# Kernel optimization log

Hardware: AMD Instinct MI355X
Metric: run time of the kernel (lower is better)

Reference implementation:

```python
import jax, jax.numpy as jnp
import numpy as np

B, N, DIN, DOUT, E, K = 64, 883, 2, 64, 10, 2
CIN = DIN + DOUT


def _dgcn(x, node_emb, time, day, speed, occupy,
          fc1_w, fc1_b, fc2_w, fc2_b, fc3_w, fc3_b, wpool, bpool):
    # x: (B, N, C); node_emb: (N, E); time/day/speed/occupy: (B, N, E)
    n = x.shape[1]
    # hyper-network filter from input features
    h = jax.nn.sigmoid(x @ fc1_w + fc1_b)
    h = jax.nn.sigmoid(h @ fc2_w + fc2_b)
    filt = h @ fc3_w + fc3_b                                  # (B, N, E)
    # dynamic node embedding: static emb modulated by time/day/speed/occupy embeddings
    dyn = node_emb[None] * time * day * speed * occupy        # (B, N, E)
    nodevec = jnp.tanh(dyn * filt)                            # (B, N, E)
    A = jax.nn.relu(jnp.einsum('bne,bme->bnm', nodevec, nodevec))  # (B, N, N)
    d = jnp.sum(A, axis=-1) ** -0.5                           # (B, N)
    I = jnp.eye(n, dtype=x.dtype)
    L = I[None] - A * d[:, :, None] * d[:, None, :]           # normalized laplacian support
    # cheb_k = 2 supports: identity and L
    x_g = jnp.stack([x, jnp.einsum('bnm,bmc->bnc', L, x)], axis=2)  # (B, N, K, C)
    weights = jnp.einsum('ne,ekio->nkio', node_emb, wpool)    # (N, K, C, O)
    bias = node_emb @ bpool                                   # (N, O)
    return jnp.einsum('bnki,nkio->bno', x_g, weights) + bias[None]


def setup_inputs() -> dict:
    key = jax.random.key(0)
    ks = jax.random.split(key, 23)
    rn = lambda k, s, sc=1.0: jax.random.normal(k, s, dtype=jnp.float32) * sc
    return dict(
        x=rn(ks[0], (B, N, DIN)),
        state=rn(ks[1], (B, N, DOUT), 0.1),
        node_embeddings=rn(ks[2], (N, E)),
        time=rn(ks[3], (B, N, E), 0.5),
        day=rn(ks[4], (B, N, E), 0.5),
        speed=rn(ks[5], (B, N, E), 0.5),
        occupy=rn(ks[6], (B, N, E), 0.5),
        gate_wpool=rn(ks[7], (E, K, CIN, 2 * DOUT), 0.1),
        gate_bpool=rn(ks[8], (E, 2 * DOUT), 0.1),
        gate_fc1_w=rn(ks[9], (CIN, 16), 0.1), gate_fc1_b=rn(ks[10], (16,), 0.1),
        gate_fc2_w=rn(ks[11], (16, 2), 0.1), gate_fc2_b=rn(ks[12], (2,), 0.1),
        gate_fc3_w=rn(ks[13], (2, E), 0.1), gate_fc3_b=rn(ks[14], (E,), 0.1),
        update_wpool=rn(ks[15], (E, K, CIN, DOUT), 0.1),
        update_bpool=rn(ks[16], (E, DOUT), 0.1),
        update_fc1_w=rn(ks[17], (CIN, 16), 0.1), update_fc1_b=rn(ks[18], (16,), 0.1),
        update_fc2_w=rn(ks[19], (16, 2), 0.1), update_fc2_b=rn(ks[20], (2,), 0.1),
        update_fc3_w=rn(ks[21], (2, E), 0.1), update_fc3_b=rn(ks[22], (E,), 0.1),
    )


def reference(x, state, node_embeddings, time, day, speed, occupy,
              gate_wpool, gate_bpool, gate_fc1_w, gate_fc1_b, gate_fc2_w,
              gate_fc2_b, gate_fc3_w, gate_fc3_b,
              update_wpool, update_bpool, update_fc1_w, update_fc1_b,
              update_fc2_w, update_fc2_b, update_fc3_w, update_fc3_b):
    xs = jnp.concatenate([x, state], axis=-1)                 # (B, N, DIN+DOUT)
    z_r = jax.nn.sigmoid(_dgcn(xs, node_embeddings, time, day, speed, occupy,
                               gate_fc1_w, gate_fc1_b, gate_fc2_w, gate_fc2_b,
                               gate_fc3_w, gate_fc3_b, gate_wpool, gate_bpool))
    z, r = jnp.split(z_r, 2, axis=-1)
    cand = jnp.concatenate([x, z * state], axis=-1)
    hc = jnp.tanh(_dgcn(cand, node_embeddings, time, day, speed, occupy,
                        update_fc1_w, update_fc1_b, update_fc2_w, update_fc2_b,
                        update_fc3_w, update_fc3_b, update_wpool, update_bpool))
    return r * state + (1.0 - r) * hc
```

## Files before the change

kernel.cpp:

```cpp
#include <hip/hip_runtime.h>
#include <cmath>

#define BB 64
#define NN 883
#define NP 896
#define EE 10
#define CC 66
#define KP 160

typedef __attribute__((ext_vector_type(8))) short bf16x8;
typedef __attribute__((ext_vector_type(4))) float f32x4;

__device__ __forceinline__ float sigmoidf_(float v) { return 1.f / (1.f + expf(-v)); }

__device__ __forceinline__ unsigned short f2bf(float f) {
  unsigned int u = __float_as_uint(f);
  u = u + 0x7FFFu + ((u >> 16) & 1u);
  return (unsigned short)(u >> 16);
}
__device__ __forceinline__ float bf2f(unsigned short h) {
  return __uint_as_float(((unsigned int)h) << 16);
}

template<int PHASE>
__global__ __launch_bounds__(256) void k1_hyper(
    const float* __restrict__ x, const float* __restrict__ state,
    const float* __restrict__ zr, const float* __restrict__ emb,
    const float* __restrict__ tme, const float* __restrict__ day,
    const float* __restrict__ spd, const float* __restrict__ occ,
    const float* __restrict__ w1, const float* __restrict__ b1,
    const float* __restrict__ w2, const float* __restrict__ b2,
    const float* __restrict__ w3, const float* __restrict__ b3,
    unsigned short* __restrict__ Acat, unsigned short* __restrict__ nvP) {
  int idx = blockIdx.x * 256 + threadIdx.x;
  if (idx >= BB * NP) return;
  int b = idx / NP, n = idx - b * NP;
  if (n >= NN) {
    *(uint4*)&nvP[(size_t)idx * 16] = make_uint4(0, 0, 0, 0);
    *(uint4*)&nvP[(size_t)idx * 16 + 8] = make_uint4(0, 0, 0, 0);
    return;
  }
  int bn = b * NN + n;

  float xsr[CC];
  xsr[0] = x[bn * 2 + 0];
  xsr[1] = x[bn * 2 + 1];
#pragma unroll
  for (int j = 0; j < 64; ++j) {
    float s = state[bn * 64 + j];
    if (PHASE == 1) s *= zr[(size_t)bn * 128 + j];
    xsr[2 + j] = s;
  }
  {
    unsigned short a16[80];
#pragma unroll
    for (int c = 0; c < CC; ++c) a16[c] = f2bf(xsr[c]);
#pragma unroll
    for (int c = CC; c < 80; ++c) a16[c] = 0;
#pragma unroll
    for (int k = 0; k < 10; ++k) {
      unsigned int w0 = (unsigned int)a16[8 * k + 0] | ((unsigned int)a16[8 * k + 1] << 16);
      unsigned int w1 = (unsigned int)a16[8 * k + 2] | ((unsigned int)a16[8 * k + 3] << 16);
      unsigned int w2_ = (unsigned int)a16[8 * k + 4] | ((unsigned int)a16[8 * k + 5] << 16);
      unsigned int w3_ = (unsigned int)a16[8 * k + 6] | ((unsigned int)a16[8 * k + 7] << 16);
      *(uint4*)&Acat[(size_t)bn * KP + 8 * k] = make_uint4(w0, w1, w2_, w3_);
    }
  }

  float h1[16];
#pragma unroll
  for (int j = 0; j < 16; ++j) h1[j] = b1[j];
#pragma unroll
  for (int i = 0; i < CC; ++i) {
    float xv = xsr[i];
#pragma unroll
    for (int j = 0; j < 16; ++j) h1[j] = fmaf(xv, w1[i * 16 + j], h1[j]);
  }
#pragma unroll
  for (int j = 0; j < 16; ++j) h1[j] = sigmoidf_(h1[j]);

  float h2[2];
#pragma unroll
  for (int j = 0; j < 2; ++j) {
    float s = b2[j];
#pragma unroll
    for (int i = 0; i < 16; ++i) s = fmaf(h1[i], w2[i * 2 + j], s);
    h2[j] = sigmoidf_(s);
  }

  unsigned short nv16[16];
#pragma unroll
  for (int e = 0; e < EE; ++e) {
    float f = b3[e] + h2[0] * w3[e] + h2[1] * w3[EE + e];
    int be = bn * EE + e;
    float dyn = emb[n * EE + e] * tme[be] * day[be] * spd[be] * occ[be];
    nv16[e] = f2bf(tanhf(dyn * f));
  }
#pragma unroll
  for (int e = EE; e < 16; ++e) nv16[e] = 0;
  unsigned int w[8];
#pragma unroll
  for (int k = 0; k < 8; ++k)
    w[k] = (unsigned int)nv16[2 * k] | ((unsigned int)nv16[2 * k + 1] << 16);
  *(uint4*)&nvP[(size_t)idx * 16]     = make_uint4(w[0], w[1], w[2], w[3]);
  *(uint4*)&nvP[(size_t)idx * 16 + 8] = make_uint4(w[4], w[5], w[6], w[7]);
}

__global__ __launch_bounds__(256) void k2_deg(const unsigned short* __restrict__ nvP,
                                              const unsigned short* __restrict__ Acat,
                                              float* __restrict__ d_g,
                                              unsigned short* __restrict__ xsdT) {
  int nt = blockIdx.x, b = blockIdx.y;
  int t = threadIdx.x, wid = t >> 6, lane = t & 63;
  int col = lane & 15, q = lane >> 4;
  int n16 = nt * 64 + wid * 16;
  __shared__ float tile[64][67];
  __shared__ float d_s[64];

  const unsigned short* nvb = nvP + (size_t)b * NP * 16;
  bf16x8 zf = {0, 0, 0, 0, 0, 0, 0, 0};
  bf16x8 anv = zf;
  if (q < 2) anv = *(const bf16x8*)&nvb[(size_t)(n16 + col) * 16 + q * 8];

  float rs[4] = {0.f, 0.f, 0.f, 0.f};
  bf16x8 cur = zf, nxt = zf;
  if (q < 2) cur = *(const bf16x8*)&nvb[(size_t)col * 16 + q * 8];
  for (int mb = 0; mb < NP; mb += 16) {
    if (q < 2 && mb + 16 < NP)
      nxt = *(const bf16x8*)&nvb[(size_t)(mb + 16 + col) * 16 + q * 8];
    f32x4 z = {0.f, 0.f, 0.f, 0.f};
    f32x4 g = __builtin_amdgcn_mfma_f32_16x16x32_bf16(anv, cur, z, 0, 0, 0);
#pragma unroll
    for (int r = 0; r < 4; ++r) rs[r] += fmaxf(g[r], 0.f);
    cur = nxt;
  }
#pragma unroll
  for (int off = 1; off < 16; off <<= 1) {
#pragma unroll
    for (int r = 0; r < 4; ++r) rs[r] += __shfl_xor(rs[r], off);
  }
  if (col == 0) {
#pragma unroll
    for (int r = 0; r < 4; ++r) {
      int n = n16 + q * 4 + r;
      float dv = (n < NN) ? rsqrtf(rs[r]) : 0.f;
      d_g[b * NP + n] = dv;
      d_s[wid * 16 + q * 4 + r] = dv;
    }
  }
  __syncthreads();

  int mb = nt * 64;
  for (int idx = t; idx < 64 * CC; idx += 256) {
    int ml = idx / CC, c = idx - ml * CC;
    int m = mb + ml;
    float v = 0.f;
    if (m < NN) v = bf2f(Acat[((size_t)(b * NN + m)) * KP + c]);
    tile[ml][c] = v * d_s[ml];
  }
  __syncthreads();
  for (int idx = t; idx < CC * 64; idx += 256) {
    int c = idx >> 6, ml = idx & 63;
    xsdT[((size_t)(b * CC) + c) * NP + mb + ml] = f2bf(tile[ml][c]);
  }
}

__global__ __launch_bounds__(256) void k3_agg(const unsigned short* __restrict__ nvP,
                                              const float* __restrict__ d_g,
                                              const unsigned short* __restrict__ xsdT,
                                              unsigned short* __restrict__ Acat) {
  int nt = blockIdx.x, b = blockIdx.y, t = threadIdx.x;
  int wid = t >> 6, lane = t & 63, col = lane & 15, q = lane >> 4;
  int n16 = nt * 64 + wid * 16;
  __shared__ __align__(16) unsigned short As[4][2][16 * 40];
  unsigned short* wAs0 = As[wid][0];
  unsigned short* wAs1 = As[wid][1];

  const unsigned short* nvb = nvP + (size_t)b * NP * 16;
  const unsigned short* xb = xsdT + (size_t)b * CC * NP;

  bf16x8 zf = {0, 0, 0, 0, 0, 0, 0, 0};
  bf16x8 anv = zf;
  if (q < 2) anv = *(const bf16x8*)&nvb[(size_t)(n16 + col) * 16 + q * 8];

  f32x4 acc[5];
#pragma unroll
  for (int ct = 0; ct < 5; ++ct) acc[ct] = (f32x4){0.f, 0.f, 0.f, 0.f};

  int cg[5];
  bool cok[5];
#pragma unroll
  for (int ct = 0; ct < 5; ++ct) { cg[ct] = ct * 16 + col; cok[ct] = cg[ct] < CC; }

  bf16x8 nv0 = zf, nv1 = zf, nv0n = zf, nv1n = zf;
  bf16x8 xs2[5], xsn[5];

  if (q < 2) {
    nv0 = *(const bf16x8*)&nvb[(size_t)(0 + col) * 16 + q * 8];
    nv1 = *(const bf16x8*)&nvb[(size_t)(16 + col) * 16 + q * 8];
  }

  {
    if (q < 2) {
      nv0n = *(const bf16x8*)&nvb[(size_t)(32 + col) * 16 + q * 8];
      nv1n = *(const bf16x8*)&nvb[(size_t)(48 + col) * 16 + q * 8];
    }
#pragma unroll
    for (int ct = 0; ct < 5; ++ct)
      xsn[ct] = cok[ct] ? *(const bf16x8*)&xb[(size_t)cg[ct] * NP + 0 + q * 8] : zf;
    f32x4 z = {0.f, 0.f, 0.f, 0.f};
    f32x4 g0 = __builtin_amdgcn_mfma_f32_16x16x32_bf16(nv0, anv, z, 0, 0, 0);
    f32x4 g1 = __builtin_amdgcn_mfma_f32_16x16x32_bf16(nv1, anv, z, 0, 0, 0);
    unsigned int a0 = (unsigned int)f2bf(fmaxf(g0[0], 0.f)) | ((unsigned int)f2bf(fmaxf(g0[1], 0.f)) << 16);
    unsigned int a1 = (unsigned int)f2bf(fmaxf(g0[2], 0.f)) | ((unsigned int)f2bf(fmaxf(g0[3], 0.f)) << 16);
    unsigned int b0 = (unsigned int)f2bf(fmaxf(g1[0], 0.f)) | ((unsigned int)f2bf(fmaxf(g1[1], 0.f)) << 16);
    unsigned int b1 = (unsigned int)f2bf(fmaxf(g1[2], 0.f)) | ((unsigned int)f2bf(fmaxf(g1[3], 0.f)) << 16);
    *(uint2*)&wAs0[col * 40 + 0 + q * 4] = make_uint2(a0, a1);
    *(uint2*)&wAs0[col * 40 + 16 + q * 4] = make_uint2(b0, b1);
    nv0 = nv0n; nv1 = nv1n;
#pragma unroll
    for (int ct = 0; ct < 5; ++ct) xs2[ct] = xsn[ct];
  }

  for (int i = 1; i < 28; ++i) {
    unsigned short* curB = (i & 1) ? wAs1 : wAs0;
    unsigned short* prvB = (i & 1) ? wAs0 : wAs1;
    bf16x8 afr = *(const bf16x8*)&prvB[col * 40 + q * 8];
    int mbn = (i + 1) * 32;
    if (i < 27 && q < 2) {
      nv0n = *(const bf16x8*)&nvb[(size_t)(mbn + col) * 16 + q * 8];
      nv1n = *(const bf16x8*)&nvb[(size_t)(mbn + 16 + col) * 16 + q * 8];
    }
    int mb = i * 32;
#pragma unroll
    for (int ct = 0; ct < 5; ++ct)
      xsn[ct] = cok[ct] ? *(const bf16x8*)&xb[(size_t)cg[ct] * NP + mb + q * 8] : zf;
    f32x4 z = {0.f, 0.f, 0.f, 0.f};
    f32x4 g0 = __builtin_amdgcn_mfma_f32_16x16x32_bf16(nv0, anv, z, 0, 0, 0);
    f32x4 g1 = __builtin_amdgcn_mfma_f32_16x16x32_bf16(nv1, anv, z, 0, 0, 0);
    unsigned int a0 = (unsigned int)f2bf(fmaxf(g0[0], 0.f)) | ((unsigned int)f2bf(fmaxf(g0[1], 0.f)) << 16);
    unsigned int a1 = (unsigned int)f2bf(fmaxf(g0[2], 0.f)) | ((unsigned int)f2bf(fmaxf(g0[3], 0.f)) << 16);
    unsigned int b0 = (unsigned int)f2bf(fmaxf(g1[0], 0.f)) | ((unsigned int)f2bf(fmaxf(g1[1], 0.f)) << 16);
    unsigned int b1 = (unsigned int)f2bf(fmaxf(g1[2], 0.f)) | ((unsigned int)f2bf(fmaxf(g1[3], 0.f)) << 16);
    *(uint2*)&curB[col * 40 + 0 + q * 4] = make_uint2(a0, a1);
    *(uint2*)&curB[col * 40 + 16 + q * 4] = make_uint2(b0, b1);
#pragma unroll
    for (int ct = 0; ct < 5; ++ct)
      acc[ct] = __builtin_amdgcn_mfma_f32_16x16x32_bf16(afr, xs2[ct], acc[ct], 0, 0, 0);
    nv0 = nv0n; nv1 = nv1n;
#pragma unroll
    for (int ct = 0; ct < 5; ++ct) xs2[ct] = xsn[ct];
  }

  {
    bf16x8 afr = *(const bf16x8*)&wAs1[col * 40 + q * 8];
#pragma unroll
    for (int ct = 0; ct < 5; ++ct)
      acc[ct] = __builtin_amdgcn_mfma_f32_16x16x32_bf16(afr, xs2[ct], acc[ct], 0, 0, 0);
  }

  float dn[4];
#pragma unroll
  for (int r = 0; r < 4; ++r) dn[r] = d_g[b * NP + n16 + q * 4 + r];
#pragma unroll
  for (int ct = 0; ct < 5; ++ct) {
    int c = ct * 16 + col;
#pragma unroll
    for (int r = 0; r < 4; ++r) {
      int n = n16 + q * 4 + r;
      if (n < NN)
        Acat[((size_t)(b * NN) + n) * KP + 80 + c] = f2bf(-(acc[ct][r] * dn[r]));
    }
  }
}

template<int OT, bool GATE>
__global__ __launch_bounds__(256) void k4b_gemm(
    const float* __restrict__ emb, const float* __restrict__ wpool,
    const float* __restrict__ bpool, const unsigned short* __restrict__ Acat,
    float* __restrict__ zr_w,
    const float* __restrict__ state, const float* __restrict__ zr_r,
    float* __restrict__ out) {
  int n = blockIdx.x, t = threadIdx.x;
  __shared__ __align__(16) unsigned short Ws[OT * 168];
  __shared__ float bias_s[OT];

  const int OG = OT / 4;
  int og = t % OG, ti = t / OG;
  int o4 = og * 4;
  float em[EE];
#pragma unroll
  for (int e = 0; e < EE; ++e) em[e] = emb[n * EE + e];

  for (int i = ti; i < CC; i += 256 / OG) {
    float4 s0 = make_float4(0.f, 0.f, 0.f, 0.f);
    float4 s1 = make_float4(0.f, 0.f, 0.f, 0.f);
#pragma unroll
    for (int e = 0; e < EE; ++e) {
      float4 w0 = *(const float4*)&wpool[(((size_t)(e * 2 + 0) * CC + i)) * OT + o4];
      float4 w1 = *(const float4*)&wpool[(((size_t)(e * 2 + 1) * CC + i)) * OT + o4];
      s0.x = fmaf(em[e], w0.x, s0.x); s0.y = fmaf(em[e], w0.y, s0.y);
      s0.z = fmaf(em[e], w0.z, s0.z); s0.w = fmaf(em[e], w0.w, s0.w);
      s1.x = fmaf(em[e], w1.x, s1.x); s1.y = fmaf(em[e], w1.y, s1.y);
      s1.z = fmaf(em[e], w1.z, s1.z); s1.w = fmaf(em[e], w1.w, s1.w);
    }
    Ws[(o4 + 0) * 168 + i] = f2bf(s0.x + s1.x);
    Ws[(o4 + 1) * 168 + i] = f2bf(s0.y + s1.y);
    Ws[(o4 + 2) * 168 + i] = f2bf(s0.z + s1.z);
    Ws[(o4 + 3) * 168 + i] = f2bf(s0.w + s1.w);
    Ws[(o4 + 0) * 168 + 80 + i] = f2bf(s1.x);
    Ws[(o4 + 1) * 168 + 80 + i] = f2bf(s1.y);
    Ws[(o4 + 2) * 168 + 80 + i] = f2bf(s1.z);
    Ws[(o4 + 3) * 168 + 80 + i] = f2bf(s1.w);
  }
  for (int idx = t; idx < OT * 14; idx += 256) {
    int o = idx / 14, kk = idx - o * 14;
    Ws[o * 168 + 66 + kk] = 0;
    Ws[o * 168 + 146 + kk] = 0;
  }
  if (t < OT) {
    float s = 0.f;
#pragma unroll
    for (int e = 0; e < EE; ++e) s = fmaf(em[e], bpool[e * OT + t], s);
    bias_s[t] = s;
  }
  __syncthreads();

  int wid = t >> 6, lane = t & 63, col = lane & 15, q = lane >> 4;
  int bA = wid * 16 + col;
  f32x4 acc[OT / 16];
#pragma unroll
  for (int ot = 0; ot < OT / 16; ++ot) acc[ot] = (f32x4){0.f, 0.f, 0.f, 0.f};

#pragma unroll
  for (int ks = 0; ks < 5; ++ks) {
    bf16x8 af = *(const bf16x8*)&Acat[((size_t)(bA * NN + n)) * KP + ks * 32 + q * 8];
#pragma unroll
    for (int ot = 0; ot < OT / 16; ++ot) {
      bf16x8 bf = *(const bf16x8*)&Ws[(ot * 16 + col) * 168 + ks * 32 + q * 8];
      acc[ot] = __builtin_amdgcn_mfma_f32_16x16x32_bf16(af, bf, acc[ot], 0, 0, 0);
    }
  }

#pragma unroll
  for (int ot = 0; ot < OT / 16; ++ot) {
    int o = ot * 16 + col;
    float bia = bias_s[o];
#pragma unroll
    for (int r = 0; r < 4; ++r) {
      int bb = wid * 16 + q * 4 + r;
      float v = acc[ot][r] + bia;
      if (GATE) {
        zr_w[((size_t)(bb * NN + n)) * 128 + o] = sigmoidf_(v);
      } else {
        float hc = tanhf(v);
        float rr = zr_r[((size_t)(bb * NN + n)) * 128 + 64 + o];
        float st = state[((size_t)(bb * NN + n)) * 64 + o];
        out[((size_t)(bb * NN + n)) * 64 + o] = fmaf(rr, st - hc, hc);
      }
    }
  }
}

extern "C" void kernel_launch(void* const* d_in, const int* in_sizes, int n_in,
                              void* d_out, int out_size, void* d_ws, size_t ws_size,
                              hipStream_t stream) {
  const float* x     = (const float*)d_in[0];
  const float* state = (const float*)d_in[1];
  const float* emb   = (const float*)d_in[2];
  const float* tme   = (const float*)d_in[3];
  const float* day   = (const float*)d_in[4];
  const float* spd   = (const float*)d_in[5];
  const float* occ   = (const float*)d_in[6];
  const float* gwp   = (const float*)d_in[7];
  const float* gbp   = (const float*)d_in[8];
  const float* gw1   = (const float*)d_in[9];
  const float* gb1   = (const float*)d_in[10];
  const float* gw2   = (const float*)d_in[11];
  const float* gb2   = (const float*)d_in[12];
  const float* gw3   = (const float*)d_in[13];
  const float* gb3   = (const float*)d_in[14];
  const float* uwp   = (const float*)d_in[15];
  const float* ubp   = (const float*)d_in[16];
  const float* uw1   = (const float*)d_in[17];
  const float* ub1   = (const float*)d_in[18];
  const float* uw2   = (const float*)d_in[19];
  const float* ub2   = (const float*)d_in[20];
  const float* uw3   = (const float*)d_in[21];
  const float* ub3   = (const float*)d_in[22];

  char* w = (char*)d_ws;
  unsigned short* Acat = (unsigned short*)w;  w += (size_t)BB * NN * KP * 2;
  unsigned short* nvP  = (unsigned short*)w;  w += (size_t)BB * NP * 16 * 2;
  unsigned short* xsdT = (unsigned short*)w;  w += (size_t)BB * CC * NP * 2;
  float* d_g  = (float*)w;  w += (size_t)BB * NP * 4;
  float* zr   = (float*)w;  w += (size_t)BB * NN * 128 * 4;

  dim3 b256(256);
  dim3 gK1((BB * NP) / 256);
  dim3 gK2(14, BB);
  dim3 gK4(NN);

  k1_hyper<0><<<gK1, b256, 0, stream>>>(x, state, zr, emb, tme, day, spd, occ,
                                        gw1, gb1, gw2, gb2, gw3, gb3, Acat, nvP);
  k2_deg<<<gK2, b256, 0, stream>>>(nvP, Acat, d_g, xsdT);
  k3_agg<<<gK2, b256, 0, stream>>>(nvP, d_g, xsdT, Acat);
  k4b_gemm<128, true><<<gK4, b256, 0, stream>>>(emb, gwp, gbp, Acat, zr,
                                                nullptr, nullptr, nullptr);
  k1_hyper<1><<<gK1, b256, 0, stream>>>(x, state, zr, emb, tme, day, spd, occ,
                                        uw1, ub1, uw2, ub2, uw3, ub3, Acat, nvP);
  k2_deg<<<gK2, b256, 0, stream>>>(nvP, Acat, d_g, xsdT);
  k3_agg<<<gK2, b256, 0, stream>>>(nvP, d_g, xsdT, Acat);
  k4b_gemm<64, false><<<gK4, b256, 0, stream>>>(emb, uwp, ubp, Acat, nullptr,
                                                state, zr, (float*)d_out);
}
```

Before: 435.4 us.

## Store node vectors and scaled features in MFMA fragment order, shuffle A tiles

Node embeddings and the degree-scaled feature matrix are now written in layouts that match the MFMA operand fragments, so k3 loads them with contiguous 16-byte vector loads and no bounds checks. The relu'd adjacency tile is moved into A-operand form with cross-lane shuffles instead of a double-buffered LDS round trip, which removes the shared memory buffer. The software prefetch of the next iteration's operands is dropped in favour of a simpler loop, so latency hiding now rests on the compiler and occupancy.

```diff
diff --git a/kernel.cpp b/kernel.cpp
--- a/kernel.cpp
+++ b/kernel.cpp
@@ -7,6 +7,8 @@
 #define EE 10
 #define CC 66
 #define KP 160
+#define NT16 56
+#define MB32 28
 
 typedef __attribute__((ext_vector_type(8))) short bf16x8;
 typedef __attribute__((ext_vector_type(4))) float f32x4;
@@ -21,6 +23,10 @@
 __device__ __forceinline__ float bf2f(unsigned short h) {
   return __uint_as_float(((unsigned int)h) << 16);
 }
+__device__ __forceinline__ unsigned int pkrelu(float a, float b) {
+  return (unsigned int)f2bf(fmaxf(a, 0.f)) | ((unsigned int)f2bf(fmaxf(b, 0.f)) << 16);
+}
+
 
 template<int PHASE>
 __global__ __launch_bounds__(256) void k1_hyper(
@@ -31,13 +37,14 @@
     const float* __restrict__ w1, const float* __restrict__ b1,
     const float* __restrict__ w2, const float* __restrict__ b2,
     const float* __restrict__ w3, const float* __restrict__ b3,
-    unsigned short* __restrict__ Acat, unsigned short* __restrict__ nvP) {
+    unsigned short* __restrict__ Acat, unsigned short* __restrict__ nv2) {
   int idx = blockIdx.x * 256 + threadIdx.x;
   if (idx >= BB * NP) return;
   int b = idx / NP, n = idx - b * NP;
+  size_t slot = ((size_t)(b * NT16 + (n >> 4)) * 32 + (n & 15) * 2) * 8;
   if (n >= NN) {
-    *(uint4*)&nvP[(size_t)idx * 16] = make_uint4(0, 0, 0, 0);
-    *(uint4*)&nvP[(size_t)idx * 16 + 8] = make_uint4(0, 0, 0, 0);
+    *(uint4*)&nv2[slot] = make_uint4(0, 0, 0, 0);
+    *(uint4*)&nv2[slot + 8] = make_uint4(0, 0, 0, 0);
     return;
   }
   int bn = b * NN + n;
@@ -59,11 +66,11 @@
     for (int c = CC; c < 80; ++c) a16[c] = 0;
 #pragma unroll
     for (int k = 0; k < 10; ++k) {
-      unsigned int w0 = (unsigned int)a16[8 * k + 0] | ((unsigned int)a16[8 * k + 1] << 16);
-      unsigned int w1 = (unsigned int)a16[8 * k + 2] | ((unsigned int)a16[8 * k + 3] << 16);
-      unsigned int w2_ = (unsigned int)a16[8 * k + 4] | ((unsigned int)a16[8 * k + 5] << 16);
-      unsigned int w3_ = (unsigned int)a16[8 * k + 6] | ((unsigned int)a16[8 * k + 7] << 16);
-      *(uint4*)&Acat[(size_t)bn * KP + 8 * k] = make_uint4(w0, w1, w2_, w3_);
+      unsigned int q0 = (unsigned int)a16[8 * k + 0] | ((unsigned int)a16[8 * k + 1] << 16);
+      unsigned int q1 = (unsigned int)a16[8 * k + 2] | ((unsigned int)a16[8 * k + 3] << 16);
+      unsigned int q2 = (unsigned int)a16[8 * k + 4] | ((unsigned int)a16[8 * k + 5] << 16);
+      unsigned int q3 = (unsigned int)a16[8 * k + 6] | ((unsigned int)a16[8 * k + 7] << 16);
+      *(uint4*)&Acat[(size_t)bn * KP + 8 * k] = make_uint4(q0, q1, q2, q3);
     }
   }
 
@@ -102,32 +109,31 @@
 #pragma unroll
   for (int k = 0; k < 8; ++k)
     w[k] = (unsigned int)nv16[2 * k] | ((unsigned int)nv16[2 * k + 1] << 16);
-  *(uint4*)&nvP[(size_t)idx * 16]     = make_uint4(w[0], w[1], w[2], w[3]);
-  *(uint4*)&nvP[(size_t)idx * 16 + 8] = make_uint4(w[4], w[5], w[6], w[7]);
-}
-
-__global__ __launch_bounds__(256) void k2_deg(const unsigned short* __restrict__ nvP,
+  *(uint4*)&nv2[slot]     = make_uint4(w[0], w[1], w[2], w[3]);
+  *(uint4*)&nv2[slot + 8] = make_uint4(w[4], w[5], w[6], w[7]);
+}
+
+__global__ __launch_bounds__(256) void k2_deg(const unsigned short* __restrict__ nv2,
                                               const unsigned short* __restrict__ Acat,
                                               float* __restrict__ d_g,
-                                              unsigned short* __restrict__ xsdT) {
+                                              unsigned short* __restrict__ xsd2) {
   int nt = blockIdx.x, b = blockIdx.y;
   int t = threadIdx.x, wid = t >> 6, lane = t & 63;
   int col = lane & 15, q = lane >> 4;
-  int n16 = nt * 64 + wid * 16;
   __shared__ float tile[64][67];
   __shared__ float d_s[64];
 
-  const unsigned short* nvb = nvP + (size_t)b * NP * 16;
+  const unsigned short* nvb = nv2 + (size_t)b * NT16 * 32 * 8;
   bf16x8 zf = {0, 0, 0, 0, 0, 0, 0, 0};
   bf16x8 anv = zf;
-  if (q < 2) anv = *(const bf16x8*)&nvb[(size_t)(n16 + col) * 16 + q * 8];
+  if (q < 2) anv = *(const bf16x8*)&nvb[((size_t)(nt * 4 + wid) * 32 + col * 2 + q) * 8];
 
   float rs[4] = {0.f, 0.f, 0.f, 0.f};
   bf16x8 cur = zf, nxt = zf;
-  if (q < 2) cur = *(const bf16x8*)&nvb[(size_t)col * 16 + q * 8];
-  for (int mb = 0; mb < NP; mb += 16) {
-    if (q < 2 && mb + 16 < NP)
-      nxt = *(const bf16x8*)&nvb[(size_t)(mb + 16 + col) * 16 + q * 8];
+  if (q < 2) cur = *(const bf16x8*)&nvb[((size_t)0 * 32 + col * 2 + q) * 8];
+  for (int mt = 0; mt < NT16; ++mt) {
+    if (q < 2 && mt + 1 < NT16)
+      nxt = *(const bf16x8*)&nvb[((size_t)(mt + 1) * 32 + col * 2 + q) * 8];
     f32x4 z = {0.f, 0.f, 0.f, 0.f};
     f32x4 g = __builtin_amdgcn_mfma_f32_16x16x32_bf16(anv, cur, z, 0, 0, 0);
 #pragma unroll
@@ -142,7 +148,7 @@
   if (col == 0) {
 #pragma unroll
     for (int r = 0; r < 4; ++r) {
-      int n = n16 + q * 4 + r;
+      int n = nt * 64 + wid * 16 + q * 4 + r;
       float dv = (n < NN) ? rsqrtf(rs[r]) : 0.f;
       d_g[b * NP + n] = dv;
       d_s[wid * 16 + q * 4 + r] = dv;
@@ -159,104 +165,80 @@
     tile[ml][c] = v * d_s[ml];
   }
   __syncthreads();
-  for (int idx = t; idx < CC * 64; idx += 256) {
-    int c = idx >> 6, ml = idx & 63;
-    xsdT[((size_t)(b * CC) + c) * NP + mb + ml] = f2bf(tile[ml][c]);
-  }
-}
-
-__global__ __launch_bounds__(256) void k3_agg(const unsigned short* __restrict__ nvP,
+  for (int idx = t; idx < 2 * 5 * 4 * 16; idx += 256) {
+    int colw = idx & 15;
+    int qw = (idx >> 4) & 3;
+    int ctw = (idx >> 6) % 5;
+    int mbbl = idx / (16 * 4 * 5);
+    unsigned int o[4];
+#pragma unroll
+    for (int jj = 0; jj < 4; ++jj) {
+      int ml = mbbl * 32 + qw * 8 + jj * 2;
+      int c = ctw * 16 + colw;
+      float v0 = (c < CC) ? tile[ml][c] : 0.f;
+      float v1 = (c < CC) ? tile[ml + 1][c] : 0.f;
+      o[jj] = (unsigned int)f2bf(v0) | ((unsigned int)f2bf(v1) << 16);
+    }
+    size_t dst = (((((size_t)b * MB32 + (nt * 2 + mbbl)) * 5 + ctw) * 4 + qw) * 16 + colw) * 8;
+    *(uint4*)&xsd2[dst] = make_uint4(o[0], o[1], o[2], o[3]);
+  }
+}
+
+__global__ __launch_bounds__(256) void k3_agg(const unsigned short* __restrict__ nv2,
                                               const float* __restrict__ d_g,
-                                              const unsigned short* __restrict__ xsdT,
+                                              const unsigned short* __restrict__ xsd2,
                                               unsigned short* __restrict__ Acat) {
   int nt = blockIdx.x, b = blockIdx.y, t = threadIdx.x;
   int wid = t >> 6, lane = t & 63, col = lane & 15, q = lane >> 4;
   int n16 = nt * 64 + wid * 16;
-  __shared__ __align__(16) unsigned short As[4][2][16 * 40];
-  unsigned short* wAs0 = As[wid][0];
-  unsigned short* wAs1 = As[wid][1];
-
-  const unsigned short* nvb = nvP + (size_t)b * NP * 16;
-  const unsigned short* xb = xsdT + (size_t)b * CC * NP;
+
+  const unsigned short* nvb = nv2 + (size_t)b * NT16 * 32 * 8;
+  const unsigned short* xb = xsd2 + (size_t)b * MB32 * 5 * 4 * 16 * 8;
 
   bf16x8 zf = {0, 0, 0, 0, 0, 0, 0, 0};
   bf16x8 anv = zf;
-  if (q < 2) anv = *(const bf16x8*)&nvb[(size_t)(n16 + col) * 16 + q * 8];
+  if (q < 2) anv = *(const bf16x8*)&nvb[((size_t)(nt * 4 + wid) * 32 + col * 2 + q) * 8];
 
   f32x4 acc[5];
 #pragma unroll
   for (int ct = 0; ct < 5; ++ct) acc[ct] = (f32x4){0.f, 0.f, 0.f, 0.f};
 
-  int cg[5];
-  bool cok[5];
-#pragma unroll
-  for (int ct = 0; ct < 5; ++ct) { cg[ct] = ct * 16 + col; cok[ct] = cg[ct] < CC; }
-
-  bf16x8 nv0 = zf, nv1 = zf, nv0n = zf, nv1n = zf;
-  bf16x8 xs2[5], xsn[5];
-
-  if (q < 2) {
-    nv0 = *(const bf16x8*)&nvb[(size_t)(0 + col) * 16 + q * 8];
-    nv1 = *(const bf16x8*)&nvb[(size_t)(16 + col) * 16 + q * 8];
-  }
-
-  {
+  int base = ((q & 1) << 5) + col;
+  bool hi = (q >= 2);
+
+  for (int i = 0; i < MB32; ++i) {
+    bf16x8 b0 = zf, b1 = zf;
     if (q < 2) {
-      nv0n = *(const bf16x8*)&nvb[(size_t)(32 + col) * 16 + q * 8];
-      nv1n = *(const bf16x8*)&nvb[(size_t)(48 + col) * 16 + q * 8];
-    }
+      b0 = *(const bf16x8*)&nvb[((size_t)(i * 2) * 32 + col * 2 + q) * 8];
+      b1 = *(const bf16x8*)&nvb[((size_t)(i * 2 + 1) * 32 + col * 2 + q) * 8];
+    }
+    bf16x8 xf[5];
 #pragma unroll
     for (int ct = 0; ct < 5; ++ct)
-      xsn[ct] = cok[ct] ? *(const bf16x8*)&xb[(size_t)cg[ct] * NP + 0 + q * 8] : zf;
+      xf[ct] = *(const bf16x8*)&xb[((((size_t)i * 5 + ct) * 4 + q) * 16 + col) * 8];
+
     f32x4 z = {0.f, 0.f, 0.f, 0.f};
-    f32x4 g0 = __builtin_amdgcn_mfma_f32_16x16x32_bf16(nv0, anv, z, 0, 0, 0);
-    f32x4 g1 = __builtin_amdgcn_mfma_f32_16x16x32_bf16(nv1, anv, z, 0, 0, 0);
-    unsigned int a0 = (unsigned int)f2bf(fmaxf(g0[0], 0.f)) | ((unsigned int)f2bf(fmaxf(g0[1], 0.f)) << 16);
-    unsigned int a1 = (unsigned int)f2bf(fmaxf(g0[2], 0.f)) | ((unsigned int)f2bf(fmaxf(g0[3], 0.f)) << 16);
-    unsigned int b0 = (unsigned int)f2bf(fmaxf(g1[0], 0.f)) | ((unsigned int)f2bf(fmaxf(g1[1], 0.f)) << 16);
-    unsigned int b1 = (unsigned int)f2bf(fmaxf(g1[2], 0.f)) | ((unsigned int)f2bf(fmaxf(g1[3], 0.f)) << 16);
-    *(uint2*)&wAs0[col * 40 + 0 + q * 4] = make_uint2(a0, a1);
-    *(uint2*)&wAs0[col * 40 + 16 + q * 4] = make_uint2(b0, b1);
-    nv0 = nv0n; nv1 = nv1n;
-#pragma unroll
-    for (int ct = 0; ct < 5; ++ct) xs2[ct] = xsn[ct];
-  }
-
-  for (int i = 1; i < 28; ++i) {
-    unsigned short* curB = (i & 1) ? wAs1 : wAs0;
-    unsigned short* prvB = (i & 1) ? wAs0 : wAs1;
-    bf16x8 afr = *(const bf16x8*)&prvB[col * 40 + q * 8];
-    int mbn = (i + 1) * 32;
-    if (i < 27 && q < 2) {
-      nv0n = *(const bf16x8*)&nvb[(size_t)(mbn + col) * 16 + q * 8];
-      nv1n = *(const bf16x8*)&nvb[(size_t)(mbn + 16 + col) * 16 + q * 8];
-    }
-    int mb = i * 32;
+    f32x4 g0 = __builtin_amdgcn_mfma_f32_16x16x32_bf16(b0, anv, z, 0, 0, 0);
+    f32x4 g1 = __builtin_amdgcn_mfma_f32_16x16x32_bf16(b1, anv, z, 0, 0, 0);
+    unsigned int p00 = pkrelu(g0[0], g0[1]), p01 = pkrelu(g0[2], g0[3]);
+    unsigned int p10 = pkrelu(g1[0], g1[1]), p11 = pkrelu(g1[2], g1[3]);
+    unsigned int s00 = (unsigned int)__shfl((int)p00, base);
+    unsigned int s01 = (unsigned int)__shfl((int)p01, base);
+    unsigned int s02 = (unsigned int)__shfl((int)p00, base + 16);
+    unsigned int s03 = (unsigned int)__shfl((int)p01, base + 16);
+    unsigned int s10 = (unsigned int)__shfl((int)p10, base);
+    unsigned int s11 = (unsigned int)__shfl((int)p11, base);
+    unsigned int s12 = (unsigned int)__shfl((int)p10, base + 16);
+    unsigned int s13 = (unsigned int)__shfl((int)p11, base + 16);
+    union { unsigned int u[4]; bf16x8 v; } cv;
+    cv.u[0] = hi ? s10 : s00;
+    cv.u[1] = hi ? s11 : s01;
+    cv.u[2] = hi ? s12 : s02;
+    cv.u[3] = hi ? s13 : s03;
+
 #pragma unroll
     for (int ct = 0; ct < 5; ++ct)
-      xsn[ct] = cok[ct] ? *(const bf16x8*)&xb[(size_t)cg[ct] * NP + mb + q * 8] : zf;
-    f32x4 z = {0.f, 0.f, 0.f, 0.f};
-    f32x4 g0 = __builtin_amdgcn_mfma_f32_16x16x32_bf16(nv0, anv, z, 0, 0, 0);
-    f32x4 g1 = __builtin_amdgcn_mfma_f32_16x16x32_bf16(nv1, anv, z, 0, 0, 0);
-    unsigned int a0 = (unsigned int)f2bf(fmaxf(g0[0], 0.f)) | ((unsigned int)f2bf(fmaxf(g0[1], 0.f)) << 16);
-    unsigned int a1 = (unsigned int)f2bf(fmaxf(g0[2], 0.f)) | ((unsigned int)f2bf(fmaxf(g0[3], 0.f)) << 16);
-    unsigned int b0 = (unsigned int)f2bf(fmaxf(g1[0], 0.f)) | ((unsigned int)f2bf(fmaxf(g1[1], 0.f)) << 16);
-    unsigned int b1 = (unsigned int)f2bf(fmaxf(g1[2], 0.f)) | ((unsigned int)f2bf(fmaxf(g1[3], 0.f)) << 16);
-    *(uint2*)&curB[col * 40 + 0 + q * 4] = make_uint2(a0, a1);
-    *(uint2*)&curB[col * 40 + 16 + q * 4] = make_uint2(b0, b1);
-#pragma unroll
-    for (int ct = 0; ct < 5; ++ct)
-      acc[ct] = __builtin_amdgcn_mfma_f32_16x16x32_bf16(afr, xs2[ct], acc[ct], 0, 0, 0);
-    nv0 = nv0n; nv1 = nv1n;
-#pragma unroll
-    for (int ct = 0; ct < 5; ++ct) xs2[ct] = xsn[ct];
-  }
-
-  {
-    bf16x8 afr = *(const bf16x8*)&wAs1[col * 40 + q * 8];
-#pragma unroll
-    for (int ct = 0; ct < 5; ++ct)
-      acc[ct] = __builtin_amdgcn_mfma_f32_16x16x32_bf16(afr, xs2[ct], acc[ct], 0, 0, 0);
+      acc[ct] = __builtin_amdgcn_mfma_f32_16x16x32_bf16(cv.v, xf[ct], acc[ct], 0, 0, 0);
   }
 
   float dn[4];
@@ -391,8 +373,8 @@
 
   char* w = (char*)d_ws;
   unsigned short* Acat = (unsigned short*)w;  w += (size_t)BB * NN * KP * 2;
-  unsigned short* nvP  = (unsigned short*)w;  w += (size_t)BB * NP * 16 * 2;
-  unsigned short* xsdT = (unsigned short*)w;  w += (size_t)BB * CC * NP * 2;
+  unsigned short* nv2  = (unsigned short*)w;  w += (size_t)BB * NT16 * 32 * 8 * 2;
+  unsigned short* xsd2 = (unsigned short*)w;  w += (size_t)BB * MB32 * 5 * 4 * 16 * 8 * 2;
   float* d_g  = (float*)w;  w += (size_t)BB * NP * 4;
   float* zr   = (float*)w;  w += (size_t)BB * NN * 128 * 4;
 
@@ -402,15 +384,15 @@
   dim3 gK4(NN);
 
   k1_hyper<0><<<gK1, b256, 0, stream>>>(x, state, zr, emb, tme, day, spd, occ,
-                                        gw1, gb1, gw2, gb2, gw3, gb3, Acat, nvP);
-  k2_deg<<<gK2, b256, 0, stream>>>(nvP, Acat, d_g, xsdT);
-  k3_agg<<<gK2, b256, 0, stream>>>(nvP, d_g, xsdT, Acat);
+                                        gw1, gb1, gw2, gb2, gw3, gb3, Acat, nv2);
+  k2_deg<<<gK2, b256, 0, stream>>>(nv2, Acat, d_g, xsd2);
+  k3_agg<<<gK2, b256, 0, stream>>>(nv2, d_g, xsd2, Acat);
   k4b_gemm<128, true><<<gK4, b256, 0, stream>>>(emb, gwp, gbp, Acat, zr,
                                                 nullptr, nullptr, nullptr);
   k1_hyper<1><<<gK1, b256, 0, stream>>>(x, state, zr, emb, tme, day, spd, occ,
-                                        uw1, ub1, uw2, ub2, uw3, ub3, Acat, nvP);
-  k2_deg<<<gK2, b256, 0, stream>>>(nvP, Acat, d_g, xsdT);
-  k3_agg<<<gK2, b256, 0, stream>>>(nvP, d_g, xsdT, Acat);
+                                        uw1, ub1, uw2, ub2, uw3, ub3, Acat, nv2);
+  k2_deg<<<gK2, b256, 0, stream>>>(nv2, Acat, d_g, xsd2);
+  k3_agg<<<gK2, b256, 0, stream>>>(nv2, d_g, xsd2, Acat);
   k4b_gemm<64, false><<<gK4, b256, 0, stream>>>(emb, uwp, ubp, Acat, nullptr,
                                                 state, zr, (float*)d_out);
 }
```

Result: faster. 355.1 us (-18.4%).
